# Performance work log

Hardware: AMD Instinct MI355X
Metric: run time of the kernel (lower is better)

The kernel has to match this reference:

```python
import jax, jax.numpy as jnp
import numpy as np

G, N, DEG = 64, 2048, 8          # graphs, nodes/graph, avg degree
NTOT = G * N                      # 131072 nodes
E = NTOT * DEG                    # 1048576 edges
K = int(np.ceil(0.2 * N))         # 410 nodes kept per graph (SAGPooling ratio=0.2)
NK = G * K                        # 26240 pooled nodes
H, C = 3, 20                      # GAT heads, per-head channels
NEG_BIG = jnp.float32(-1e30)


def gcn(x, src, dst, W, b, n):
    """PyG GCNConv: x' = D^-1/2 (A+I) D^-1/2 x W + b (edge weight 1)."""
    h = x @ W
    deg = jax.ops.segment_sum(jnp.ones(src.shape[0], x.dtype), dst, num_segments=n) + 1.0
    dinv = jax.lax.rsqrt(deg)
    coef = dinv[src] * dinv[dst]                    # [E]
    agg = jax.ops.segment_sum(h[src] * coef[:, None], dst, num_segments=n)
    agg = agg + h * (dinv * dinv)[:, None]          # self loops
    return agg + b


def setup_inputs() -> dict:
    key = jax.random.key(0)
    ks = jax.random.split(key, 16)
    # edges constrained within each graph: per-graph local indices + offsets
    off = jnp.repeat(jnp.arange(G, dtype=jnp.int32) * N, N * DEG)   # [E]
    src = jax.random.randint(ks[0], (E,), 0, N, dtype=jnp.int32) + off
    dst = jax.random.randint(ks[1], (E,), 0, N, dtype=jnp.int32) + off
    batch = jnp.repeat(jnp.arange(G, dtype=jnp.int32), N)           # [NTOT]
    x = jax.random.normal(ks[2], (NTOT, 5), jnp.float32)
    s = 0.1
    return {
        "x": x, "src": src, "dst": dst, "batch": batch,
        "W1": jax.random.normal(ks[3], (5, 10)) * s,   "b1": jnp.zeros((10,)),
        "Ws": jax.random.normal(ks[4], (10, 1)) * s,   "bs": jnp.zeros((1,)),
        "Wg": jax.random.normal(ks[5], (10, H * C)) * s,
        "a_src": jax.random.normal(ks[6], (H, C)) * s,
        "a_dst": jax.random.normal(ks[7], (H, C)) * s,
        "bg": jnp.zeros((H * C,)),
        "Wf1": jax.random.normal(ks[8], (60, 30)) * s, "bf1": jnp.zeros((30,)),
        "Wf2": jax.random.normal(ks[9], (30, 3)) * s,  "bf2": jnp.zeros((3,)),
    }


def reference(x, src, dst, batch, W1, b1, Ws, bs, Wg, a_src, a_dst, bg, Wf1, bf1, Wf2, bf2):
    n = x.shape[0]
    # GCNConv(5,10)
    x1 = gcn(x, src, dst, W1, b1, n)                              # [NTOT,10]
    # SAGPooling: GCN scorer, top-k per graph, gate by tanh(score)
    score = gcn(x1, src, dst, Ws, bs, n)[:, 0]                    # [NTOT]
    _, topi = jax.lax.top_k(score.reshape(G, N), K)               # [G,K]
    perm = (topi + (jnp.arange(G) * N)[:, None]).reshape(-1)      # [NK] global ids
    xp = x1[perm] * jnp.tanh(score[perm])[:, None]                # [NK,10]
    # remap edges; drop (mask) edges touching removed nodes (filter_adj)
    new_idx = jnp.full((n,), -1, jnp.int32).at[perm].set(jnp.arange(NK, dtype=jnp.int32))
    s2, d2 = new_idx[src], new_idx[dst]
    emask = (s2 >= 0) & (d2 >= 0)
    s2 = jnp.where(emask, s2, 0)
    d2 = jnp.where(emask, d2, 0)
    # GATConv(10, 20, heads=3) with self loops
    h = (xp @ Wg).reshape(NK, H, C)
    al_s = jnp.sum(h * a_src, -1)                                 # [NK,H]
    al_d = jnp.sum(h * a_dst, -1)
    loop = jnp.arange(NK, dtype=jnp.int32)
    sa = jnp.concatenate([s2, loop])
    da = jnp.concatenate([d2, loop])
    ma = jnp.concatenate([emask, jnp.ones((NK,), bool)])
    logits = jax.nn.leaky_relu(al_s[sa] + al_d[da], 0.2)          # [E+NK,H]
    logits = jnp.where(ma[:, None], logits, NEG_BIG)
    mx = jax.ops.segment_max(logits, da, num_segments=NK)         # finite: self loops
    w = jnp.exp(logits - mx[da]) * ma[:, None]
    denom = jax.ops.segment_sum(w, da, num_segments=NK)
    alpha = w / denom[da]                                         # edge softmax
    out = jax.ops.segment_sum(h[sa] * alpha[..., None], da, num_segments=NK)  # [NK,H,C]
    xg = out.reshape(NK, H * C) + bg                              # concat heads -> 60
    # scatter_add readout over graphs
    g = jax.ops.segment_sum(xg, batch[perm], num_segments=G)      # [G,60]
    # MLP + LogSoftmax
    z = jax.nn.relu(g @ Wf1 + bf1) @ Wf2 + bf2                    # [G,3]
    return jax.nn.log_softmax(z, axis=1)
```

## Files before the change

kernel.cpp:

```cpp
#include <hip/hip_runtime.h>
#include <math.h>

#define G    64
#define NPG  2048
#define NTOT (G * NPG)
#define EPG  (NPG * 8)
#define KSEL 410
#define NH   3
#define NC   20
#define HC   60
#define FCAP 24
#define KPAD 512
#define RP   12

#define OFF_H1P   0
#define OFF_XP    0
#define OFF_FADJ  16400
#define OFF_FCNT  36080
#define OFF_HF    37728
#define OFF_CSR   98304
#define OFF_HIST  131072
#define OFF_RS    139264
#define OFF_ALS   139264
#define OFF_ALD   144184
#define OFF_SK    147456
#define OFF_WRED  149104
#define OFF_GOUT  151024
#define OFF_HID   151264
#define OFF_NEWL  155648
#define OFF_PERML 159744
#define OFF_WSUM  160568
#define OFF_FLAGS 160632
#define ARENA_SZ  160648

__device__ inline float leaky(float x) { return x >= 0.f ? x : 0.2f * x; }

__device__ inline int wave_incl_scan(int v) {
    int lane = threadIdx.x & 63;
#pragma unroll
    for (int d = 1; d < 64; d <<= 1) {
        int t = __shfl_up(v, d, 64);
        if (lane >= d) v += t;
    }
    return v;
}

__global__ __launch_bounds__(1024) void k_all(
    const float* __restrict__ x, const int* __restrict__ src, const int* __restrict__ dst,
    const float* __restrict__ W1, const float* __restrict__ b1,
    const float* __restrict__ Ws, const float* __restrict__ bs,
    const float* __restrict__ Wg, const float* __restrict__ a_srcw,
    const float* __restrict__ a_dstw, const float* __restrict__ bg,
    const float* __restrict__ Wf1, const float* __restrict__ bf1,
    const float* __restrict__ Wf2, const float* __restrict__ bf2,
    float* __restrict__ out)
{
    __shared__ __align__(16) char arena[ARENA_SZ];
    float*          h1p   = (float*)(arena + OFF_H1P);
    float*          xpL   = (float*)(arena + OFF_XP);
    unsigned short* fadjL = (unsigned short*)(arena + OFF_FADJ);
    int*            fcntL = (int*)(arena + OFF_FCNT);
    float*          hfL   = (float*)(arena + OFF_HF);
    unsigned short* csrL  = (unsigned short*)(arena + OFF_CSR);
    int*            hist  = (int*)(arena + OFF_HIST);
    int*            rsL   = (int*)(arena + OFF_RS);
    float*          alsL  = (float*)(arena + OFF_ALS);
    float*          aldL  = (float*)(arena + OFF_ALD);
    unsigned*       skL   = (unsigned*)(arena + OFF_SK);
    float*          wred  = (float*)(arena + OFF_WRED);
    float*          goutL = (float*)(arena + OFF_GOUT);
    float*          hidL  = (float*)(arena + OFF_HID);
    unsigned short* newLs = (unsigned short*)(arena + OFF_NEWL);
    unsigned short* permL = (unsigned short*)(arena + OFF_PERML);
    int*            wsumL = (int*)(arena + OFF_WSUM);
    int*            flags = (int*)(arena + OFF_FLAGS);
#define bselS  flags[0]
#define bneedS flags[1]
#define totS   flags[3]

    int g = blockIdx.x, tid = threadIdx.x, wid = tid >> 6;
    int nbase = g * NPG, ebase = g * EPG;

    for (int i = tid; i < NPG; i += 1024) hist[i] = 0;
    for (int i = tid; i < NPG; i += 1024) {
        float xi[5];
#pragma unroll
        for (int k = 0; k < 5; k++) xi[k] = x[(size_t)(nbase + i) * 5 + k];
        float v[10];
#pragma unroll
        for (int j = 0; j < 10; j++) {
            float s = 0.f;
#pragma unroll
            for (int k = 0; k < 5; k++) s += xi[k] * W1[k * 10 + j];
            v[j] = s;
        }
        float4* row = (float4*)(h1p + i * RP);
        row[0] = make_float4(v[0], v[1], v[2], v[3]);
        row[1] = make_float4(v[4], v[5], v[6], v[7]);
        row[2] = make_float4(v[8], v[9], 0.f, 0.f);
    }
    __syncthreads();
    for (int e = tid; e < EPG; e += 1024)
        atomicAdd(&hist[dst[ebase + e] - nbase], 1);
    __syncthreads();
    {
        int b2 = tid * 2;
        int v0 = hist[b2], v1 = hist[b2 + 1];
        int s = v0 + v1;
        int incl = wave_incl_scan(s);
        if ((tid & 63) == 63) wsumL[wid] = incl;
        __syncthreads();
        if (tid == 0) {
            int a = 0;
#pragma unroll
            for (int w = 0; w < 16; w++) { int t = wsumL[w]; wsumL[w] = a; a += t; }
        }
        __syncthreads();
        int base = wsumL[wid] + incl - s;
        rsL[b2] = base;
        rsL[b2 + 1] = base + v0;
        h1p[b2 * RP + 10] = rsqrtf((float)v0 + 1.0f);
        h1p[(b2 + 1) * RP + 10] = rsqrtf((float)v1 + 1.0f);
        hist[b2] = 0; hist[b2 + 1] = 0;
    }
    __syncthreads();
    for (int e = tid; e < EPG; e += 1024) {
        int ee = ebase + e;
        int sl = src[ee] - nbase;
        int dl = dst[ee] - nbase;
        int pos = rsL[dl] + atomicAdd(&hist[dl], 1);
        csrL[pos] = (unsigned short)sl;
    }
    __syncthreads();

    {
        int i0 = tid, i1 = tid + 1024;
        int e0 = rsL[i0], e0e = rsL[i0 + 1];
        int e1 = rsL[i1], e1e = (i1 == NPG - 1) ? EPG : rsL[i1 + 1];
        float acc0[10], acc1[10];
#pragma unroll
        for (int j = 0; j < 10; j++) { acc0[j] = 0.f; acc1[j] = 0.f; }
        while (e0 < e0e || e1 < e1e) {
            if (e0 < e0e) {
                int s = csrL[e0++];
                const float4* rw = (const float4*)(h1p + s * RP);
                float4 r0 = rw[0], r1 = rw[1], r2 = rw[2];
                float dv = r2.z;
                acc0[0] += r0.x * dv; acc0[1] += r0.y * dv; acc0[2] += r0.z * dv; acc0[3] += r0.w * dv;
                acc0[4] += r1.x * dv; acc0[5] += r1.y * dv; acc0[6] += r1.z * dv; acc0[7] += r1.w * dv;
                acc0[8] += r2.x * dv; acc0[9] += r2.y * dv;
            }
            if (e1 < e1e) {
                int s = csrL[e1++];
                const float4* rw = (const float4*)(h1p + s * RP);
                float4 r0 = rw[0], r1 = rw[1], r2 = rw[2];
                float dv = r2.z;
                acc1[0] += r0.x * dv; acc1[1] += r0.y * dv; acc1[2] += r0.z * dv; acc1[3] += r0.w * dv;
                acc1[4] += r1.x * dv; acc1[5] += r1.y * dv; acc1[6] += r1.z * dv; acc1[7] += r1.w * dv;
                acc1[8] += r2.x * dv; acc1[9] += r2.y * dv;
            }
        }
        const float4* q0 = (const float4*)(h1p + i0 * RP);
        const float4* q1 = (const float4*)(h1p + i1 * RP);
        float4 s00 = q0[0], s01 = q0[1], s02 = q0[2];
        float4 s10 = q1[0], s11 = q1[1], s12 = q1[2];
        float di0 = s02.z, d20 = di0 * di0;
        float di1 = s12.z, d21 = di1 * di1;
        float b1r[10];
#pragma unroll
        for (int j = 0; j < 10; j++) b1r[j] = b1[j];
        float v0[10], v1[10];
        v0[0] = acc0[0] * di0 + s00.x * d20 + b1r[0];
        v0[1] = acc0[1] * di0 + s00.y * d20 + b1r[1];
        v0[2] = acc0[2] * di0 + s00.z * d20 + b1r[2];
        v0[3] = acc0[3] * di0 + s00.w * d20 + b1r[3];
        v0[4] = acc0[4] * di0 + s01.x * d20 + b1r[4];
        v0[5] = acc0[5] * di0 + s01.y * d20 + b1r[5];
        v0[6] = acc0[6] * di0 + s01.z * d20 + b1r[6];
        v0[7] = acc0[7] * di0 + s01.w * d20 + b1r[7];
        v0[8] = acc0[8] * di0 + s02.x * d20 + b1r[8];
        v0[9] = acc0[9] * di0 + s02.y * d20 + b1r[9];
        v1[0] = acc1[0] * di1 + s10.x * d21 + b1r[0];
        v1[1] = acc1[1] * di1 + s10.y * d21 + b1r[1];
        v1[2] = acc1[2] * di1 + s10.z * d21 + b1r[2];
        v1[3] = acc1[3] * di1 + s10.w * d21 + b1r[3];
        v1[4] = acc1[4] * di1 + s11.x * d21 + b1r[4];
        v1[5] = acc1[5] * di1 + s11.y * d21 + b1r[5];
        v1[6] = acc1[6] * di1 + s11.z * d21 + b1r[6];
        v1[7] = acc1[7] * di1 + s11.w * d21 + b1r[7];
        v1[8] = acc1[8] * di1 + s12.x * d21 + b1r[8];
        v1[9] = acc1[9] * di1 + s12.y * d21 + b1r[9];
        float hs0 = 0.f, hs1 = 0.f;
#pragma unroll
        for (int j = 0; j < 10; j++) { float w = Ws[j]; hs0 += v0[j] * w; hs1 += v1[j] * w; }
        __syncthreads();
        float4* w0 = (float4*)(h1p + i0 * RP);
        w0[0] = make_float4(v0[0], v0[1], v0[2], v0[3]);
        w0[1] = make_float4(v0[4], v0[5], v0[6], v0[7]);
        w0[2] = make_float4(v0[8], v0[9], di0, hs0);
        float4* w1 = (float4*)(h1p + i1 * RP);
        w1[0] = make_float4(v1[0], v1[1], v1[2], v1[3]);
        w1[1] = make_float4(v1[4], v1[5], v1[6], v1[7]);
        w1[2] = make_float4(v1[8], v1[9], di1, hs1);
    }
    __syncthreads();

    {
        float bsv = bs[0];
        int i0 = tid, i1 = tid + 1024;
        float2 own0 = *(const float2*)(h1p + i0 * RP + 10);
        float2 own1 = *(const float2*)(h1p + i1 * RP + 10);
        int e0 = rsL[i0], e0e = rsL[i0 + 1];
        int e1 = rsL[i1], e1e = (i1 == NPG - 1) ? EPG : rsL[i1 + 1];
        float a0 = 0.f, a1 = 0.f;
        while (e0 < e0e || e1 < e1e) {
            if (e0 < e0e) { float2 dh = *(const float2*)(h1p + csrL[e0++] * RP + 10); a0 += dh.x * dh.y; }
            if (e1 < e1e) { float2 dh = *(const float2*)(h1p + csrL[e1++] * RP + 10); a1 += dh.x * dh.y; }
        }
        float sc0 = own0.x * a0 + own0.y * own0.x * own0.x + bsv;
        float sc1 = own1.x * a1 + own1.y * own1.x * own1.x + bsv;
        unsigned u0 = __float_as_uint(sc0);
        unsigned u1 = __float_as_uint(sc1);
        skL[i0] = (u0 & 0x80000000u) ? ~u0 : (u0 | 0x80000000u);
        skL[i1] = (u1 & 0x80000000u) ? ~u1 : (u1 | 0x80000000u);
        newLs[i0] = 0xFFFFu; newLs[i1] = 0xFFFFu;
        hist[i0] = 0; hist[i1] = 0;
    }
    int need = KSEL;
    unsigned prefix = 0;
    __syncthreads();

    for (int lv = 0; lv < 3; lv++) {
        for (int i = tid; i < NPG; i += 1024) {
            unsigned k = skL[i];
            bool match; unsigned bb;
            if (lv == 0)      { match = true;                  bb = k >> 21; }
            else if (lv == 1) { match = ((k >> 21) == prefix); bb = (k >> 10) & 0x7FFu; }
            else              { match = ((k >> 10) == prefix); bb = k & 0x3FFu; }
            if (match) atomicAdd(&hist[bb], 1);
        }
        __syncthreads();
        int b2 = tid * 2;
        int v0 = hist[b2], v1 = hist[b2 + 1];
        hist[b2] = 0; hist[b2 + 1] = 0;
        int s = v0 + v1;
        int incl = wave_incl_scan(s);
        if ((tid & 63) == 63) wsumL[wid] = incl;
        __syncthreads();
        if (tid == 0) {
            int a = 0;
#pragma unroll
            for (int w = 0; w < 16; w++) { int t = wsumL[w]; wsumL[w] = a; a += t; }
            totS = a;
        }
        __syncthreads();
        int base = wsumL[wid] + incl - s;
        int tot = totS;
        { int Sb = tot - base;        int Sb1 = Sb - v0; if (Sb >= need && Sb1 < need) { bselS = b2;     bneedS = need - Sb1; } }
        { int Sb = tot - (base + v0); int Sb1 = Sb - v1; if (Sb >= need && Sb1 < need) { bselS = b2 + 1; bneedS = need - Sb1; } }
        __syncthreads();
        if (lv == 0)      prefix = (unsigned)bselS;
        else if (lv == 1) prefix = (prefix << 11) | (unsigned)bselS;
        else              prefix = (prefix << 10) | (unsigned)bselS;
        need = bneedS;
        __syncthreads();
    }
    unsigned T = prefix;
    int greaterCnt = KSEL - need;

    {
        int b2 = tid * 2;
        unsigned k0 = skL[b2], k1 = skL[b2 + 1];
        int gt0 = k0 > T ? 1 : 0, gt1 = k1 > T ? 1 : 0;
        int eq0 = k0 == T ? 1 : 0, eq1 = k1 == T ? 1 : 0;
        int pack = ((gt0 + gt1) << 16) | (eq0 + eq1);
        int incl = wave_incl_scan(pack);
        if ((tid & 63) == 63) wsumL[wid] = incl;
        __syncthreads();
        if (tid == 0) {
            int a = 0;
#pragma unroll
            for (int w = 0; w < 16; w++) { int t = wsumL[w]; wsumL[w] = a; a += t; }
        }
        __syncthreads();
        int base = wsumL[wid] + incl - pack;
        int gb = base >> 16, eb = base & 0xFFFF;
        if (gt0) { permL[gb] = (unsigned short)b2; newLs[b2] = (unsigned short)gb; }
        if (gt1) { int r = gb + gt0; permL[r] = (unsigned short)(b2 + 1); newLs[b2 + 1] = (unsigned short)r; }
        if (eq0 && eb < need) { int p = greaterCnt + eb; permL[p] = (unsigned short)b2; newLs[b2] = (unsigned short)p; }
        if (eq1) { int r = eb + eq0; if (r < need) { int p = greaterCnt + r; permL[p] = (unsigned short)(b2 + 1); newLs[b2 + 1] = (unsigned short)p; } }
    }
    __syncthreads();

    {
        float4 rq0, rq1, rq2; float tt = 0.f;
        bool havep = (tid < KSEL);
        if (havep) {
            int iL = permL[tid];
            unsigned k = skL[iL];
            unsigned u = (k & 0x80000000u) ? (k & 0x7FFFFFFFu) : ~k;
            tt = tanhf(__uint_as_float(u));
            const float4* xr = (const float4*)(h1p + iL * RP);
            rq0 = xr[0]; rq1 = xr[1]; rq2 = xr[2];
        }
        __syncthreads();
        if (havep) {
            float* xp = xpL + tid * 10;
            xp[0] = rq0.x * tt; xp[1] = rq0.y * tt; xp[2] = rq0.z * tt; xp[3] = rq0.w * tt;
            xp[4] = rq1.x * tt; xp[5] = rq1.y * tt; xp[6] = rq1.z * tt; xp[7] = rq1.w * tt;
            xp[8] = rq2.x * tt; xp[9] = rq2.y * tt;
        }
    }
    __syncthreads();

    for (int p = tid; p < KSEL; p += 1024) {
        int iL = permL[p];
        int p0 = rsL[iL], p1 = (iL == NPG - 1) ? EPG : rsL[iL + 1];
        int c = 0;
        int e = p0;
        while (e < p1) {
            int n = p1 - e; n = n > 8 ? 8 : n;
            int b8[8];
#pragma unroll
            for (int j = 0; j < 8; j++) b8[j] = csrL[e + (j < n ? j : 0)];
            unsigned short n8[8];
#pragma unroll
            for (int j = 0; j < 8; j++) n8[j] = newLs[b8[j]];
#pragma unroll
            for (int j = 0; j < 8; j++)
                if (j < n && n8[j] != 0xFFFFu && c < FCAP) fadjL[p * FCAP + c++] = n8[j];
            e += n;
        }
        fcntL[p] = c;
    }
    __syncthreads();

    for (int t = tid; t < KSEL * NH; t += 1024) {
        int p = t / NH, hh = t - p * NH;
        float xi[10];
#pragma unroll
        for (int k = 0; k < 10; k++) xi[k] = xpL[p * 10 + k];
        float v[NC];
        float as_ = 0.f, ad_ = 0.f;
#pragma unroll
        for (int c = 0; c < NC; c++) {
            int j = hh * NC + c;
            float vv = 0.f;
#pragma unroll
            for (int k = 0; k < 10; k++) vv += xi[k] * Wg[k * HC + j];
            v[c] = vv;
            as_ += vv * a_srcw[j];
            ad_ += vv * a_dstw[j];
        }
        float4* hr = (float4*)(hfL + p * HC + hh * NC);
#pragma unroll
        for (int q = 0; q < 5; q++)
            hr[q] = make_float4(v[4 * q], v[4 * q + 1], v[4 * q + 2], v[4 * q + 3]);
        alsL[p * NH + hh] = as_;
        aldL[p * NH + hh] = ad_;
    }
    __syncthreads();

    {
        float res[NC];
#pragma unroll
        for (int rnd = 0; rnd < 2; rnd++) {
            int task = rnd == 0 ? tid : 1024 + tid;
            bool on = rnd == 0 || tid < KPAD;
            int hh = task >> 9, p = task & (KPAD - 1);
            if (on) {
                if (p < KSEL) {
                    float aldp = aldL[p * NH + hh];
                    float lself = leaky(alsL[p * NH + hh] + aldp);
                    int c = fcntL[p];
                    const float4* hp = (const float4*)(hfL + p * HC + hh * NC);
                    float4 r0 = hp[0], r1 = hp[1], r2 = hp[2], r3 = hp[3], r4 = hp[4];
                    float wsum = 1.f;
#pragma unroll
                    for (int e = 0; e < FCAP; e++) {
                        if (e < c) {
                            int idx = fadjL[p * FCAP + e];
                            float w = __expf(leaky(alsL[idx * NH + hh] + aldp) - lself);
                            wsum += w;
                            const float4* hq = (const float4*)(hfL + idx * HC + hh * NC);
                            float4 t0 = hq[0], t1 = hq[1], t2 = hq[2], t3 = hq[3], t4 = hq[4];
                            r0.x += w * t0.x; r0.y += w * t0.y; r0.z += w * t0.z; r0.w += w * t0.w;
                            r1.x += w * t1.x; r1.y += w * t1.y; r1.z += w * t1.z; r1.w += w * t1.w;
                            r2.x += w * t2.x; r2.y += w * t2.y; r2.z += w * t2.z; r2.w += w * t2.w;
                            r3.x += w * t3.x; r3.y += w * t3.y; r3.z += w * t3.z; r3.w += w * t3.w;
                            r4.x += w * t4.x; r4.y += w * t4.y; r4.z += w * t4.z; r4.w += w * t4.w;
                        }
                    }
                    float inv = 1.f / wsum;
                    res[0] = r0.x * inv;  res[1] = r0.y * inv;  res[2] = r0.z * inv;  res[3] = r0.w * inv;
                    res[4] = r1.x * inv;  res[5] = r1.y * inv;  res[6] = r1.z * inv;  res[7] = r1.w * inv;
                    res[8] = r2.x * inv;  res[9] = r2.y * inv;  res[10] = r2.z * inv; res[11] = r2.w * inv;
                    res[12] = r3.x * inv; res[13] = r3.y * inv; res[14] = r3.z * inv; res[15] = r3.w * inv;
                    res[16] = r4.x * inv; res[17] = r4.y * inv; res[18] = r4.z * inv; res[19] = r4.w * inv;
                } else {
#pragma unroll
                    for (int cc = 0; cc < NC; cc++) res[cc] = 0.f;
                }
#pragma unroll
                for (int cc = 0; cc < NC; cc++) {
                    float v = res[cc];
#pragma unroll
                    for (int d = 1; d < 64; d <<= 1) v += __shfl_xor(v, d, 64);
                    res[cc] = v;
                }
                if ((tid & 63) == 0) {
                    int slot = rnd == 0 ? hh * 8 + (wid & 7) : 16 + wid;
#pragma unroll
                    for (int cc = 0; cc < NC; cc++) wred[slot * NC + cc] = res[cc];
                }
            }
        }
    }
    __syncthreads();
    if (tid < HC) {
        int hh = tid / NC, c = tid - hh * NC;
        float a = 0.f;
#pragma unroll
        for (int w = 0; w < 8; w++) a += wred[(hh * 8 + w) * NC + c];
        goutL[tid] = a + (float)KSEL * bg[tid];
    }
    __syncthreads();

    if (tid < 30) {
        float s = bf1[tid];
#pragma unroll
        for (int k = 0; k < HC; k++) s += goutL[k] * Wf1[k * 30 + tid];
        hidL[tid] = s > 0.f ? s : 0.f;
    }
    __syncthreads();
    if (tid == 0) {
        float z[3];
#pragma unroll
        for (int j = 0; j < 3; j++) {
            float s = bf2[j];
            for (int k = 0; k < 30; k++) s += hidL[k] * Wf2[k * 3 + j];
            z[j] = s;
        }
        float m = fmaxf(z[0], fmaxf(z[1], z[2]));
        float lse = logf(expf(z[0] - m) + expf(z[1] - m) + expf(z[2] - m)) + m;
#pragma unroll
        for (int j = 0; j < 3; j++) out[g * 3 + j] = z[j] - lse;
    }
}

extern "C" void kernel_launch(void* const* d_in, const int* in_sizes, int n_in,
                              void* d_out, int out_size, void* d_ws, size_t ws_size,
                              hipStream_t stream) {
    const float* x     = (const float*)d_in[0];
    const int*   src   = (const int*)d_in[1];
    const int*   dst   = (const int*)d_in[2];
    const float* W1    = (const float*)d_in[4];
    const float* b1    = (const float*)d_in[5];
    const float* Ws    = (const float*)d_in[6];
    const float* bs    = (const float*)d_in[7];
    const float* Wg    = (const float*)d_in[8];
    const float* a_src = (const float*)d_in[9];
    const float* a_dst = (const float*)d_in[10];
    const float* bg    = (const float*)d_in[11];
    const float* Wf1   = (const float*)d_in[12];
    const float* bf1   = (const float*)d_in[13];
    const float* Wf2   = (const float*)d_in[14];
    const float* bf2   = (const float*)d_in[15];
    float* out = (float*)d_out;
    (void)d_ws; (void)ws_size;

    k_all<<<G, 1024, 0, stream>>>(x, src, dst, W1, b1, Ws, bs, Wg, a_src, a_dst,
                                  bg, Wf1, bf1, Wf2, bf2, out);
}
```

Baseline: 141.4 us.

## Switch node feature and GAT feature tiles in LDS from row-major to planar layout

Stores the per-node GCN features, degree norm and score in planar (structure-of-arrays) LDS layout instead of 12-float padded rows, and likewise stores GAT head features channel-major. The goal is fewer LDS bank conflicts on the random-neighbour gathers. The cost is that each gather becomes scalar 4-byte loads instead of float4 loads. The GAT edge loop also switches from a fixed unrolled FCAP loop to a dynamic loop bounded by the real count.

```diff
diff --git a/kernel.cpp b/kernel.cpp
--- a/kernel.cpp
+++ b/kernel.cpp
@@ -11,9 +11,8 @@
 #define HC   60
 #define FCAP 24
 #define KPAD 512
-#define RP   12
-
-#define OFF_H1P   0
+
+#define OFF_PLN   0
 #define OFF_XP    0
 #define OFF_FADJ  16400
 #define OFF_FCNT  36080
@@ -33,6 +32,8 @@
 #define OFF_FLAGS 160632
 #define ARENA_SZ  160648
 
+#define PL(j, i) h1T[((j) << 11) + (i)]
+
 __device__ inline float leaky(float x) { return x >= 0.f ? x : 0.2f * x; }
 
 __device__ inline int wave_incl_scan(int v) {
@@ -56,7 +57,7 @@
     float* __restrict__ out)
 {
     __shared__ __align__(16) char arena[ARENA_SZ];
-    float*          h1p   = (float*)(arena + OFF_H1P);
+    float*          h1T   = (float*)(arena + OFF_PLN);
     float*          xpL   = (float*)(arena + OFF_XP);
     unsigned short* fadjL = (unsigned short*)(arena + OFF_FADJ);
     int*            fcntL = (int*)(arena + OFF_FCNT);
@@ -86,18 +87,13 @@
         float xi[5];
 #pragma unroll
         for (int k = 0; k < 5; k++) xi[k] = x[(size_t)(nbase + i) * 5 + k];
-        float v[10];
 #pragma unroll
         for (int j = 0; j < 10; j++) {
             float s = 0.f;
 #pragma unroll
             for (int k = 0; k < 5; k++) s += xi[k] * W1[k * 10 + j];
-            v[j] = s;
-        }
-        float4* row = (float4*)(h1p + i * RP);
-        row[0] = make_float4(v[0], v[1], v[2], v[3]);
-        row[1] = make_float4(v[4], v[5], v[6], v[7]);
-        row[2] = make_float4(v[8], v[9], 0.f, 0.f);
+            PL(j, i) = s;
+        }
     }
     __syncthreads();
     for (int e = tid; e < EPG; e += 1024)
@@ -119,8 +115,8 @@
         int base = wsumL[wid] + incl - s;
         rsL[b2] = base;
         rsL[b2 + 1] = base + v0;
-        h1p[b2 * RP + 10] = rsqrtf((float)v0 + 1.0f);
-        h1p[(b2 + 1) * RP + 10] = rsqrtf((float)v1 + 1.0f);
+        PL(10, b2)     = rsqrtf((float)v0 + 1.0f);
+        PL(10, b2 + 1) = rsqrtf((float)v1 + 1.0f);
         hist[b2] = 0; hist[b2 + 1] = 0;
     }
     __syncthreads();
@@ -143,82 +139,56 @@
         while (e0 < e0e || e1 < e1e) {
             if (e0 < e0e) {
                 int s = csrL[e0++];
-                const float4* rw = (const float4*)(h1p + s * RP);
-                float4 r0 = rw[0], r1 = rw[1], r2 = rw[2];
-                float dv = r2.z;
-                acc0[0] += r0.x * dv; acc0[1] += r0.y * dv; acc0[2] += r0.z * dv; acc0[3] += r0.w * dv;
-                acc0[4] += r1.x * dv; acc0[5] += r1.y * dv; acc0[6] += r1.z * dv; acc0[7] += r1.w * dv;
-                acc0[8] += r2.x * dv; acc0[9] += r2.y * dv;
+                float dv = PL(10, s);
+#pragma unroll
+                for (int j = 0; j < 10; j++) acc0[j] += PL(j, s) * dv;
             }
             if (e1 < e1e) {
                 int s = csrL[e1++];
-                const float4* rw = (const float4*)(h1p + s * RP);
-                float4 r0 = rw[0], r1 = rw[1], r2 = rw[2];
-                float dv = r2.z;
-                acc1[0] += r0.x * dv; acc1[1] += r0.y * dv; acc1[2] += r0.z * dv; acc1[3] += r0.w * dv;
-                acc1[4] += r1.x * dv; acc1[5] += r1.y * dv; acc1[6] += r1.z * dv; acc1[7] += r1.w * dv;
-                acc1[8] += r2.x * dv; acc1[9] += r2.y * dv;
+                float dv = PL(10, s);
+#pragma unroll
+                for (int j = 0; j < 10; j++) acc1[j] += PL(j, s) * dv;
             }
         }
-        const float4* q0 = (const float4*)(h1p + i0 * RP);
-        const float4* q1 = (const float4*)(h1p + i1 * RP);
-        float4 s00 = q0[0], s01 = q0[1], s02 = q0[2];
-        float4 s10 = q1[0], s11 = q1[1], s12 = q1[2];
-        float di0 = s02.z, d20 = di0 * di0;
-        float di1 = s12.z, d21 = di1 * di1;
+        float s0[10], s1[10];
+#pragma unroll
+        for (int j = 0; j < 10; j++) { s0[j] = PL(j, i0); s1[j] = PL(j, i1); }
+        float di0 = PL(10, i0), d20 = di0 * di0;
+        float di1 = PL(10, i1), d21 = di1 * di1;
         float b1r[10];
 #pragma unroll
         for (int j = 0; j < 10; j++) b1r[j] = b1[j];
         float v0[10], v1[10];
-        v0[0] = acc0[0] * di0 + s00.x * d20 + b1r[0];
-        v0[1] = acc0[1] * di0 + s00.y * d20 + b1r[1];
-        v0[2] = acc0[2] * di0 + s00.z * d20 + b1r[2];
-        v0[3] = acc0[3] * di0 + s00.w * d20 + b1r[3];
-        v0[4] = acc0[4] * di0 + s01.x * d20 + b1r[4];
-        v0[5] = acc0[5] * di0 + s01.y * d20 + b1r[5];
-        v0[6] = acc0[6] * di0 + s01.z * d20 + b1r[6];
-        v0[7] = acc0[7] * di0 + s01.w * d20 + b1r[7];
-        v0[8] = acc0[8] * di0 + s02.x * d20 + b1r[8];
-        v0[9] = acc0[9] * di0 + s02.y * d20 + b1r[9];
-        v1[0] = acc1[0] * di1 + s10.x * d21 + b1r[0];
-        v1[1] = acc1[1] * di1 + s10.y * d21 + b1r[1];
-        v1[2] = acc1[2] * di1 + s10.z * d21 + b1r[2];
-        v1[3] = acc1[3] * di1 + s10.w * d21 + b1r[3];
-        v1[4] = acc1[4] * di1 + s11.x * d21 + b1r[4];
-        v1[5] = acc1[5] * di1 + s11.y * d21 + b1r[5];
-        v1[6] = acc1[6] * di1 + s11.z * d21 + b1r[6];
-        v1[7] = acc1[7] * di1 + s11.w * d21 + b1r[7];
-        v1[8] = acc1[8] * di1 + s12.x * d21 + b1r[8];
-        v1[9] = acc1[9] * di1 + s12.y * d21 + b1r[9];
+#pragma unroll
+        for (int j = 0; j < 10; j++) {
+            v0[j] = acc0[j] * di0 + s0[j] * d20 + b1r[j];
+            v1[j] = acc1[j] * di1 + s1[j] * d21 + b1r[j];
+        }
         float hs0 = 0.f, hs1 = 0.f;
 #pragma unroll
         for (int j = 0; j < 10; j++) { float w = Ws[j]; hs0 += v0[j] * w; hs1 += v1[j] * w; }
         __syncthreads();
-        float4* w0 = (float4*)(h1p + i0 * RP);
-        w0[0] = make_float4(v0[0], v0[1], v0[2], v0[3]);
-        w0[1] = make_float4(v0[4], v0[5], v0[6], v0[7]);
-        w0[2] = make_float4(v0[8], v0[9], di0, hs0);
-        float4* w1 = (float4*)(h1p + i1 * RP);
-        w1[0] = make_float4(v1[0], v1[1], v1[2], v1[3]);
-        w1[1] = make_float4(v1[4], v1[5], v1[6], v1[7]);
-        w1[2] = make_float4(v1[8], v1[9], di1, hs1);
+#pragma unroll
+        for (int j = 0; j < 10; j++) { PL(j, i0) = v0[j]; PL(j, i1) = v1[j]; }
+        PL(11, i0) = hs0;
+        PL(11, i1) = hs1;
     }
     __syncthreads();
 
     {
         float bsv = bs[0];
         int i0 = tid, i1 = tid + 1024;
-        float2 own0 = *(const float2*)(h1p + i0 * RP + 10);
-        float2 own1 = *(const float2*)(h1p + i1 * RP + 10);
+        float di0 = PL(10, i0), hsO0 = PL(11, i0);
+        float di1 = PL(10, i1), hsO1 = PL(11, i1);
         int e0 = rsL[i0], e0e = rsL[i0 + 1];
         int e1 = rsL[i1], e1e = (i1 == NPG - 1) ? EPG : rsL[i1 + 1];
         float a0 = 0.f, a1 = 0.f;
         while (e0 < e0e || e1 < e1e) {
-            if (e0 < e0e) { float2 dh = *(const float2*)(h1p + csrL[e0++] * RP + 10); a0 += dh.x * dh.y; }
-            if (e1 < e1e) { float2 dh = *(const float2*)(h1p + csrL[e1++] * RP + 10); a1 += dh.x * dh.y; }
-        }
-        float sc0 = own0.x * a0 + own0.y * own0.x * own0.x + bsv;
-        float sc1 = own1.x * a1 + own1.y * own1.x * own1.x + bsv;
+            if (e0 < e0e) { int s = csrL[e0++]; a0 += PL(10, s) * PL(11, s); }
+            if (e1 < e1e) { int s = csrL[e1++]; a1 += PL(10, s) * PL(11, s); }
+        }
+        float sc0 = di0 * a0 + hsO0 * di0 * di0 + bsv;
+        float sc1 = di1 * a1 + hsO1 * di1 * di1 + bsv;
         unsigned u0 = __float_as_uint(sc0);
         unsigned u1 = __float_as_uint(sc1);
         skL[i0] = (u0 & 0x80000000u) ? ~u0 : (u0 | 0x80000000u);
@@ -293,22 +263,21 @@
     __syncthreads();
 
     {
-        float4 rq0, rq1, rq2; float tt = 0.f;
+        float rq[10]; float tt = 0.f;
         bool havep = (tid < KSEL);
         if (havep) {
             int iL = permL[tid];
             unsigned k = skL[iL];
             unsigned u = (k & 0x80000000u) ? (k & 0x7FFFFFFFu) : ~k;
             tt = tanhf(__uint_as_float(u));
-            const float4* xr = (const float4*)(h1p + iL * RP);
-            rq0 = xr[0]; rq1 = xr[1]; rq2 = xr[2];
+#pragma unroll
+            for (int j = 0; j < 10; j++) rq[j] = PL(j, iL);
         }
         __syncthreads();
         if (havep) {
             float* xp = xpL + tid * 10;
-            xp[0] = rq0.x * tt; xp[1] = rq0.y * tt; xp[2] = rq0.z * tt; xp[3] = rq0.w * tt;
-            xp[4] = rq1.x * tt; xp[5] = rq1.y * tt; xp[6] = rq1.z * tt; xp[7] = rq1.w * tt;
-            xp[8] = rq2.x * tt; xp[9] = rq2.y * tt;
+#pragma unroll
+            for (int j = 0; j < 10; j++) xp[j] = rq[j] * tt;
         }
     }
     __syncthreads();
@@ -340,7 +309,6 @@
         float xi[10];
 #pragma unroll
         for (int k = 0; k < 10; k++) xi[k] = xpL[p * 10 + k];
-        float v[NC];
         float as_ = 0.f, ad_ = 0.f;
 #pragma unroll
         for (int c = 0; c < NC; c++) {
@@ -348,14 +316,10 @@
             float vv = 0.f;
 #pragma unroll
             for (int k = 0; k < 10; k++) vv += xi[k] * Wg[k * HC + j];
-            v[c] = vv;
+            hfL[j * KSEL + p] = vv;
             as_ += vv * a_srcw[j];
             ad_ += vv * a_dstw[j];
         }
-        float4* hr = (float4*)(hfL + p * HC + hh * NC);
-#pragma unroll
-        for (int q = 0; q < 5; q++)
-            hr[q] = make_float4(v[4 * q], v[4 * q + 1], v[4 * q + 2], v[4 * q + 3]);
         alsL[p * NH + hh] = as_;
         aldL[p * NH + hh] = ad_;
     }
@@ -373,30 +337,21 @@
                     float aldp = aldL[p * NH + hh];
                     float lself = leaky(alsL[p * NH + hh] + aldp);
                     int c = fcntL[p];
-                    const float4* hp = (const float4*)(hfL + p * HC + hh * NC);
-                    float4 r0 = hp[0], r1 = hp[1], r2 = hp[2], r3 = hp[3], r4 = hp[4];
+                    const float* hb = hfL + (hh * NC) * KSEL;
+                    float r[NC];
+#pragma unroll
+                    for (int cc = 0; cc < NC; cc++) r[cc] = hb[cc * KSEL + p];
                     float wsum = 1.f;
-#pragma unroll
-                    for (int e = 0; e < FCAP; e++) {
-                        if (e < c) {
-                            int idx = fadjL[p * FCAP + e];
-                            float w = __expf(leaky(alsL[idx * NH + hh] + aldp) - lself);
-                            wsum += w;
-                            const float4* hq = (const float4*)(hfL + idx * HC + hh * NC);
-                            float4 t0 = hq[0], t1 = hq[1], t2 = hq[2], t3 = hq[3], t4 = hq[4];
-                            r0.x += w * t0.x; r0.y += w * t0.y; r0.z += w * t0.z; r0.w += w * t0.w;
-                            r1.x += w * t1.x; r1.y += w * t1.y; r1.z += w * t1.z; r1.w += w * t1.w;
-                            r2.x += w * t2.x; r2.y += w * t2.y; r2.z += w * t2.z; r2.w += w * t2.w;
-                            r3.x += w * t3.x; r3.y += w * t3.y; r3.z += w * t3.z; r3.w += w * t3.w;
-                            r4.x += w * t4.x; r4.y += w * t4.y; r4.z += w * t4.z; r4.w += w * t4.w;
-                        }
+                    for (int e = 0; e < c; e++) {
+                        int idx = fadjL[p * FCAP + e];
+                        float w = __expf(leaky(alsL[idx * NH + hh] + aldp) - lself);
+                        wsum += w;
+#pragma unroll
+                        for (int cc = 0; cc < NC; cc++) r[cc] += w * hb[cc * KSEL + idx];
                     }
                     float inv = 1.f / wsum;
-                    res[0] = r0.x * inv;  res[1] = r0.y * inv;  res[2] = r0.z * inv;  res[3] = r0.w * inv;
-                    res[4] = r1.x * inv;  res[5] = r1.y * inv;  res[6] = r1.z * inv;  res[7] = r1.w * inv;
-                    res[8] = r2.x * inv;  res[9] = r2.y * inv;  res[10] = r2.z * inv; res[11] = r2.w * inv;
-                    res[12] = r3.x * inv; res[13] = r3.y * inv; res[14] = r3.z * inv; res[15] = r3.w * inv;
-                    res[16] = r4.x * inv; res[17] = r4.y * inv; res[18] = r4.z * inv; res[19] = r4.w * inv;
+#pragma unroll
+                    for (int cc = 0; cc < NC; cc++) res[cc] = r[cc] * inv;
                 } else {
 #pragma unroll
                     for (int cc = 0; cc < NC; cc++) res[cc] = 0.f;
```

After: 150.3 us. 6.3% more time.
